# Kernel tuning notes

Measured on AMD Instinct MI355X. Metric: run time of the kernel, lower is better.

Reference implementation:

```python
import jax, jax.numpy as jnp
import numpy as np

N_NODES = 100000
N_EDGES = 1200000
EMBED_DIM = 64
N_LAYERS = 3


def setup_inputs() -> dict:
    key = jax.random.key(0)
    k1, k2, k3, k4 = jax.random.split(key, 4)
    embeddings = jax.random.normal(k1, (N_NODES, EMBED_DIM), dtype=jnp.float32)
    edge_weight = jax.random.uniform(k2, (N_EDGES,), dtype=jnp.float32)
    edge_src = jax.random.randint(k3, (N_EDGES,), 0, N_NODES, dtype=jnp.int32)
    edge_dst = jax.random.randint(k4, (N_EDGES,), 0, N_NODES, dtype=jnp.int32)
    return {"embeddings": embeddings, "edge_weight": edge_weight,
            "edge_src": edge_src, "edge_dst": edge_dst}


def _spmm(edge_src, edge_dst, edge_weight, x):
    # (A @ x)[d] = sum_{e: dst(e)=d} w[e] * x[src(e)]  -- COO SpMM via gather + segment_sum
    msgs = edge_weight[:, None] * x[edge_src]  # [E, D]
    return jax.ops.segment_sum(msgs, edge_dst, num_segments=N_NODES)


def reference(embeddings, edge_weight, edge_src, edge_dst):
    all_embeddings = [embeddings]
    ego = embeddings
    for _ in range(N_LAYERS):
        ego = _spmm(edge_src, edge_dst, edge_weight, ego)
        all_embeddings.append(ego)
    # stack layer outputs: [n_layers+1, N, D]
    return jnp.stack(all_embeddings, axis=0)
```

## Files before the change

kernel.cpp:

```cpp
#include <hip/hip_runtime.h>
#include <hip/hip_fp16.h>


#define N_NODES 100000
#define DIM 64
#define SCAN_CHUNK 1024

#define NR 8
#define RSIZE ((N_NODES + NR - 1) / NR)
#define SLICES 256

typedef int   vint4   __attribute__((ext_vector_type(4)));
typedef float vfloat4 __attribute__((ext_vector_type(4)));

union HU { unsigned u; __half2 h; };

__global__ void convert_kernel(const float* __restrict__ emb, float* __restrict__ out0,
                               unsigned short* __restrict__ xh0, int n8) {
    int i = blockIdx.x * blockDim.x + threadIdx.x;
    if (i >= n8) return;
    const vfloat4* e4 = (const vfloat4*)emb;
    vfloat4 a = __builtin_nontemporal_load(e4 + 2 * i);
    vfloat4 b = __builtin_nontemporal_load(e4 + 2 * i + 1);
    vfloat4* o4 = (vfloat4*)out0;
    __builtin_nontemporal_store(a, o4 + 2 * i);
    __builtin_nontemporal_store(b, o4 + 2 * i + 1);
    HU c0, c1, c2, c3;
    c0.h = __float22half2_rn(make_float2(a[0], a[1]));
    c1.h = __float22half2_rn(make_float2(a[2], a[3]));
    c2.h = __float22half2_rn(make_float2(b[0], b[1]));
    c3.h = __float22half2_rn(make_float2(b[2], b[3]));
    vint4 p = { (int)c0.u, (int)c1.u, (int)c2.u, (int)c3.u };
    ((vint4*)xh0)[i] = p;
}


__global__ void hist_kernel(const int* __restrict__ edst, int* __restrict__ deg, int E) {
    int i = blockIdx.x * blockDim.x + threadIdx.x;
    int nv = E >> 2;
    if (i < nv) {
        vint4 d = __builtin_nontemporal_load(((const vint4*)edst) + i);
        atomicAdd(&deg[d[0]], 1);
        atomicAdd(&deg[d[1]], 1);
        atomicAdd(&deg[d[2]], 1);
        atomicAdd(&deg[d[3]], 1);
    }
    if (i == 0) {
        for (int e = nv << 2; e < E; ++e) atomicAdd(&deg[edst[e]], 1);
    }
}

__global__ void scan1_kernel(const int* __restrict__ src, int* __restrict__ dst,
                             int* __restrict__ bsum, int n) {
    __shared__ int sdata[256];
    int tid = threadIdx.x;
    int base = blockIdx.x * SCAN_CHUNK + tid * 4;
    int v[4];
    #pragma unroll
    for (int i = 0; i < 4; ++i) v[i] = (base + i < n) ? src[base + i] : 0;
    int tsum = v[0] + v[1] + v[2] + v[3];
    sdata[tid] = tsum;
    __syncthreads();
    for (int d = 1; d < 256; d <<= 1) {
        int t = (tid >= d) ? sdata[tid - d] : 0;
        __syncthreads();
        sdata[tid] += t;
        __syncthreads();
    }
    int excl = sdata[tid] - tsum;
    if (tid == 255) bsum[blockIdx.x] = sdata[255];
    int run = excl;
    #pragma unroll
    for (int i = 0; i < 4; ++i) {
        if (base + i < n) dst[base + i] = run;
        run += v[i];
    }
}

__global__ void scan2_kernel(int* __restrict__ bsum, int nb) {
    __shared__ int s[128];
    int tid = threadIdx.x;
    int v = (tid < nb) ? bsum[tid] : 0;
    s[tid] = v;
    __syncthreads();
    for (int d = 1; d < 128; d <<= 1) {
        int t = (tid >= d) ? s[tid - d] : 0;
        __syncthreads();
        s[tid] += t;
        __syncthreads();
    }
    if (tid < nb) bsum[tid] = s[tid] - v;
}

__global__ void scan3_kernel(int* __restrict__ off, int* __restrict__ cur,
                             const int* __restrict__ bsum, int n) {
    int i = blockIdx.x * blockDim.x + threadIdx.x;
    if (i < n) {
        int v = off[i] + bsum[i / SCAN_CHUNK];
        off[i] = v;
        cur[i] = v;
    }
}

__global__ void scatter_range_kernel(const int* __restrict__ esrc, const int* __restrict__ edst,
                                     const float* __restrict__ ew, int* __restrict__ cur,
                                     int2* __restrict__ pairs, int E, int chunk) {
    const int r = blockIdx.x & (NR - 1);
    const int s = blockIdx.x / NR;
    const int lo = r * RSIZE;
    const int hi = min(lo + RSIZE, N_NODES);
    const int e0 = s * chunk;
    if (e0 >= E) return;
    const int e1 = min(e0 + chunk, E);
    const int nv = (e1 - e0) >> 2;
    const vint4*   s4 = (const vint4*)(esrc + e0);
    const vint4*   d4 = (const vint4*)(edst + e0);
    const vfloat4* w4 = (const vfloat4*)(ew + e0);
    for (int i = threadIdx.x; i < nv; i += blockDim.x) {
        vint4 dd = __builtin_nontemporal_load(d4 + i);
        vint4 ss = __builtin_nontemporal_load(s4 + i);
        vfloat4 ww = __builtin_nontemporal_load(w4 + i);
        #pragma unroll
        for (int j = 0; j < 4; ++j) {
            int dj = dd[j];
            if (dj >= lo && dj < hi) {
                int p = atomicAdd(&cur[dj], 1);
                int2 pr;
                pr.x = ss[j];
                pr.y = __float_as_int(ww[j]);
                pairs[p] = pr;
            }
        }
    }
    for (int e = e0 + (nv << 2) + threadIdx.x; e < e1; e += blockDim.x) {
        int dj = edst[e];
        if (dj >= lo && dj < hi) {
            int p = atomicAdd(&cur[dj], 1);
            int2 pr;
            pr.x = esrc[e];
            pr.y = __float_as_int(ew[e]);
            pairs[p] = pr;
        }
    }
}


__global__ void spmm_h_kernel(const unsigned short* __restrict__ xh,
                              const int2* __restrict__ pairs,
                              const int* __restrict__ off,
                              const int* __restrict__ deg,
                              float* __restrict__ y,
                              unsigned short* __restrict__ yh) {
    int gtid = blockIdx.x * blockDim.x + threadIdx.x;
    int node = gtid >> 6;
    int lane = threadIdx.x & 63;
    int o  = lane >> 3;
    int ol = lane & 7;
    if (node >= N_NODES) return;
    int s0 = off[node];
    int n  = deg[node];
    float a0 = 0.f, a1 = 0.f, a2 = 0.f, a3 = 0.f;
    float a4 = 0.f, a5 = 0.f, a6 = 0.f, a7 = 0.f;
    for (int k = o; k < n; k += 8) {
        int2 pr = pairs[s0 + k];
        float w = __int_as_float(pr.y);
        const vint4* row = (const vint4*)(xh + (size_t)pr.x * DIM);
        vint4 v = row[ol];
        HU c; float2 f;
        c.u = (unsigned)v[0]; f = __half22float2(c.h); a0 += w * f.x; a1 += w * f.y;
        c.u = (unsigned)v[1]; f = __half22float2(c.h); a2 += w * f.x; a3 += w * f.y;
        c.u = (unsigned)v[2]; f = __half22float2(c.h); a4 += w * f.x; a5 += w * f.y;
        c.u = (unsigned)v[3]; f = __half22float2(c.h); a6 += w * f.x; a7 += w * f.y;
    }
    #pragma unroll
    for (int d = 8; d <= 32; d <<= 1) {
        a0 += __shfl_xor(a0, d); a1 += __shfl_xor(a1, d);
        a2 += __shfl_xor(a2, d); a3 += __shfl_xor(a3, d);
        a4 += __shfl_xor(a4, d); a5 += __shfl_xor(a5, d);
        a6 += __shfl_xor(a6, d); a7 += __shfl_xor(a7, d);
    }
    if (o == 0) {
        float* yr = y + (size_t)node * DIM + ol * 8;
        vfloat4 r0 = { a0, a1, a2, a3 };
        vfloat4 r1 = { a4, a5, a6, a7 };
        __builtin_nontemporal_store(r0, (vfloat4*)yr);
        __builtin_nontemporal_store(r1, (vfloat4*)yr + 1);
        HU c0, c1, c2, c3;
        c0.h = __float22half2_rn(make_float2(a0, a1));
        c1.h = __float22half2_rn(make_float2(a2, a3));
        c2.h = __float22half2_rn(make_float2(a4, a5));
        c3.h = __float22half2_rn(make_float2(a6, a7));
        vint4 p = { (int)c0.u, (int)c1.u, (int)c2.u, (int)c3.u };
        *((vint4*)(yh + (size_t)node * DIM + ol * 8)) = p;
    }
}


__global__ void spmm_csr_kernel(const float* __restrict__ x,
                                const int2* __restrict__ pairs,
                                const int* __restrict__ off,
                                const int* __restrict__ deg,
                                float* __restrict__ y) {
    int gtid = blockIdx.x * blockDim.x + threadIdx.x;
    int node = gtid >> 6;
    int lane = threadIdx.x & 63;
    int o  = lane >> 3;
    int ol = lane & 7;
    if (node >= N_NODES) return;
    int s0 = off[node];
    int n  = deg[node];
    float4 a0 = make_float4(0.f, 0.f, 0.f, 0.f);
    float4 a1 = a0;
    for (int k = o; k < n; k += 8) {
        int2 pr = pairs[s0 + k];
        float w = __int_as_float(pr.y);
        const float4* row = (const float4*)(x + (size_t)pr.x * DIM);
        float4 v0 = row[ol];
        float4 v1 = row[ol + 8];
        a0.x += w * v0.x; a0.y += w * v0.y; a0.z += w * v0.z; a0.w += w * v0.w;
        a1.x += w * v1.x; a1.y += w * v1.y; a1.z += w * v1.z; a1.w += w * v1.w;
    }
    #pragma unroll
    for (int d = 8; d <= 32; d <<= 1) {
        a0.x += __shfl_xor(a0.x, d); a0.y += __shfl_xor(a0.y, d);
        a0.z += __shfl_xor(a0.z, d); a0.w += __shfl_xor(a0.w, d);
        a1.x += __shfl_xor(a1.x, d); a1.y += __shfl_xor(a1.y, d);
        a1.z += __shfl_xor(a1.z, d); a1.w += __shfl_xor(a1.w, d);
    }
    if (o == 0) {
        vfloat4* yrow = (vfloat4*)(y + (size_t)node * DIM);
        vfloat4 r0 = { a0.x, a0.y, a0.z, a0.w };
        vfloat4 r1 = { a1.x, a1.y, a1.z, a1.w };
        __builtin_nontemporal_store(r0, yrow + ol);
        __builtin_nontemporal_store(r1, yrow + ol + 8);
    }
}


__global__ void spmm_atomic_kernel(const float* __restrict__ x, const float* __restrict__ ew,
                                   const int* __restrict__ esrc, const int* __restrict__ edst,
                                   float* __restrict__ y, int n_edges) {
    long long tid = (long long)blockIdx.x * blockDim.x + threadIdx.x;
    int e = (int)(tid >> 6);
    int d = (int)(tid & 63);
    if (e >= n_edges) return;
    int s = esrc[e]; int t = edst[e]; float w = ew[e];
    atomicAdd(&y[(long long)t * DIM + d], w * x[(long long)s * DIM + d]);
}

extern "C" void kernel_launch(void* const* d_in, const int* in_sizes, int n_in,
                              void* d_out, int out_size, void* d_ws, size_t ws_size,
                              hipStream_t stream) {
    const float* emb  = (const float*)d_in[0];
    const float* ew   = (const float*)d_in[1];
    const int*   esrc = (const int*)d_in[2];
    const int*   edst = (const int*)d_in[3];
    float* out = (float*)d_out;

    const int E = in_sizes[1];
    const size_t layer_elems = (size_t)N_NODES * DIM;

    const size_t need_h   = (size_t)E * 8 + 2 * layer_elems * 2 + (size_t)3 * N_NODES * 4 + 1024;
    const size_t need_f32 = (size_t)E * 8 + (size_t)3 * N_NODES * 4 + 1024;

    if (ws_size >= need_h && E >= 4) {
        char* w = (char*)d_ws;
        int2* pairs = (int2*)w;
        unsigned short* xh0 = (unsigned short*)(w + (size_t)E * 8);
        unsigned short* xh1 = xh0 + layer_elems;
        int* deg  = (int*)(xh1 + layer_elems);
        int* cur  = deg + N_NODES;
        int* off  = cur + N_NODES;
        int* bsum = off + N_NODES;

        hipMemsetAsync(deg, 0, (size_t)N_NODES * 4, stream);

        const int n8 = (int)(layer_elems / 8);
        convert_kernel<<<(n8 + 255) / 256, 256, 0, stream>>>(emb, out, xh0, n8);

        const int nv4 = E >> 2;
        hist_kernel<<<(nv4 + 255) / 256, 256, 0, stream>>>(edst, deg, E);

        const int nscan = (N_NODES + SCAN_CHUNK - 1) / SCAN_CHUNK;
        scan1_kernel<<<nscan, 256, 0, stream>>>(deg, off, bsum, N_NODES);
        scan2_kernel<<<1, 128, 0, stream>>>(bsum, nscan);
        scan3_kernel<<<(N_NODES + 255) / 256, 256, 0, stream>>>(off, cur, bsum, N_NODES);

        const int chunk = (((E + SLICES - 1) / SLICES) + 3) & ~3;
        scatter_range_kernel<<<NR * SLICES, 256, 0, stream>>>(esrc, edst, ew, cur, pairs, E, chunk);

        const int nb = (N_NODES + 3) / 4;
        unsigned short* xs[2] = { xh0, xh1 };
        for (int l = 1; l <= 3; ++l) {
            spmm_h_kernel<<<nb, 256, 0, stream>>>(
                xs[(l - 1) & 1], pairs, off, deg,
                out + (size_t)l * layer_elems, xs[l & 1]);
        }
    } else if (ws_size >= need_f32 && E >= 4) {
        char* w = (char*)d_ws;
        int2* pairs = (int2*)w;
        int* deg  = (int*)(w + (size_t)E * 8);
        int* cur  = deg + N_NODES;
        int* off  = cur + N_NODES;
        int* bsum = off + N_NODES;

        hipMemcpyAsync(out, emb, layer_elems * sizeof(float), hipMemcpyDeviceToDevice, stream);
        hipMemsetAsync(deg, 0, (size_t)N_NODES * 4, stream);
        const int nv4 = E >> 2;
        hist_kernel<<<(nv4 + 255) / 256, 256, 0, stream>>>(edst, deg, E);
        const int nscan = (N_NODES + SCAN_CHUNK - 1) / SCAN_CHUNK;
        scan1_kernel<<<nscan, 256, 0, stream>>>(deg, off, bsum, N_NODES);
        scan2_kernel<<<1, 128, 0, stream>>>(bsum, nscan);
        scan3_kernel<<<(N_NODES + 255) / 256, 256, 0, stream>>>(off, cur, bsum, N_NODES);
        const int chunk = (((E + SLICES - 1) / SLICES) + 3) & ~3;
        scatter_range_kernel<<<NR * SLICES, 256, 0, stream>>>(esrc, edst, ew, cur, pairs, E, chunk);
        const int nb = (N_NODES + 3) / 4;
        for (int l = 1; l <= 3; ++l) {
            spmm_csr_kernel<<<nb, 256, 0, stream>>>(
                out + (size_t)(l - 1) * layer_elems, pairs, off, deg,
                out + (size_t)l * layer_elems);
        }
    } else {
        hipMemcpyAsync(out, emb, layer_elems * sizeof(float), hipMemcpyDeviceToDevice, stream);
        hipMemsetAsync(out + layer_elems, 0, 3 * layer_elems * sizeof(float), stream);
        const long long total_threads = (long long)E * 64;
        const int blocks = (int)((total_threads + 255) / 256);
        for (int l = 1; l <= 3; ++l) {
            spmm_atomic_kernel<<<blocks, 256, 0, stream>>>(
                out + (size_t)(l - 1) * layer_elems, ew, esrc, edst,
                out + (size_t)l * layer_elems, E);
        }
    }
}
```

Before: 369.9 us.

## Replace range-filtered CSR scatter with two-pass radix partition of edges

The CSR build previously had every destination-range block rescan the whole edge list, reading edges once per range. Now the histogram also records per-block range counts, those are scanned, and partA writes edges into a temp buffer bucketed by range with src and local dst packed into one word. partB then scatters each bucket into final CSR positions. This cuts redundant edge reads but adds a temp buffer, an extra pass, and a packing limit on node ids.

```diff
diff --git a/kernel.cpp b/kernel.cpp
--- a/kernel.cpp
+++ b/kernel.cpp
@@ -8,9 +8,12 @@
 
 #define NR 8
 #define RSIZE ((N_NODES + NR - 1) / NR)
+#define NBLK 256
+#define PBR 32
 #define SLICES 256
 
 typedef int   vint4   __attribute__((ext_vector_type(4)));
+typedef int   vint2   __attribute__((ext_vector_type(2)));
 typedef float vfloat4 __attribute__((ext_vector_type(4)));
 
 union HU { unsigned u; __half2 h; };
@@ -35,19 +38,33 @@
 }
 
 
-__global__ void hist_kernel(const int* __restrict__ edst, int* __restrict__ deg, int E) {
-    int i = blockIdx.x * blockDim.x + threadIdx.x;
-    int nv = E >> 2;
-    if (i < nv) {
-        vint4 d = __builtin_nontemporal_load(((const vint4*)edst) + i);
-        atomicAdd(&deg[d[0]], 1);
-        atomicAdd(&deg[d[1]], 1);
-        atomicAdd(&deg[d[2]], 1);
-        atomicAdd(&deg[d[3]], 1);
-    }
-    if (i == 0) {
-        for (int e = nv << 2; e < E; ++e) atomicAdd(&deg[edst[e]], 1);
-    }
+__global__ void hist_part_kernel(const int* __restrict__ edst, int* __restrict__ deg,
+                                 int* __restrict__ cntT, int E, int chunk) {
+    __shared__ int lcnt[NR];
+    if (threadIdx.x < NR) lcnt[threadIdx.x] = 0;
+    __syncthreads();
+    const int b = blockIdx.x;
+    const int e0 = b * chunk;
+    const int e1 = min(e0 + chunk, E);
+    if (e0 < E) {
+        const int nv = (e1 - e0) >> 2;
+        const vint4* d4 = (const vint4*)(edst + e0);
+        for (int i = threadIdx.x; i < nv; i += blockDim.x) {
+            vint4 d = __builtin_nontemporal_load(d4 + i);
+            #pragma unroll
+            for (int j = 0; j < 4; ++j) {
+                atomicAdd(&deg[d[j]], 1);
+                atomicAdd(&lcnt[d[j] / RSIZE], 1);
+            }
+        }
+        for (int e = e0 + (nv << 2) + threadIdx.x; e < e1; e += blockDim.x) {
+            int d = edst[e];
+            atomicAdd(&deg[d], 1);
+            atomicAdd(&lcnt[d / RSIZE], 1);
+        }
+    }
+    __syncthreads();
+    if (threadIdx.x < NR) cntT[threadIdx.x * NBLK + b] = lcnt[threadIdx.x];
 }
 
 __global__ void scan1_kernel(const int* __restrict__ src, int* __restrict__ dst,
@@ -77,19 +94,23 @@
     }
 }
 
-__global__ void scan2_kernel(int* __restrict__ bsum, int nb) {
-    __shared__ int s[128];
-    int tid = threadIdx.x;
-    int v = (tid < nb) ? bsum[tid] : 0;
-    s[tid] = v;
+__global__ void scan2b_kernel(int* __restrict__ a, int nb) {
+    __shared__ int s[1024];
+    int t = threadIdx.x;
+    int i0 = 2 * t, i1 = 2 * t + 1;
+    int v0 = (i0 < nb) ? a[i0] : 0;
+    int v1 = (i1 < nb) ? a[i1] : 0;
+    s[t] = v0 + v1;
     __syncthreads();
-    for (int d = 1; d < 128; d <<= 1) {
-        int t = (tid >= d) ? s[tid - d] : 0;
+    for (int d = 1; d < 1024; d <<= 1) {
+        int tt = (t >= d) ? s[t - d] : 0;
         __syncthreads();
-        s[tid] += t;
+        s[t] += tt;
         __syncthreads();
     }
-    if (tid < nb) bsum[tid] = s[tid] - v;
+    int excl = s[t] - (v0 + v1);
+    if (i0 < nb) a[i0] = excl;
+    if (i1 < nb) a[i1] = excl + v0;
 }
 
 __global__ void scan3_kernel(int* __restrict__ off, int* __restrict__ cur,
@@ -99,6 +120,138 @@
         int v = off[i] + bsum[i / SCAN_CHUNK];
         off[i] = v;
         cur[i] = v;
+    }
+}
+
+__global__ void partA_kernel(const int* __restrict__ esrc, const int* __restrict__ edst,
+                             const float* __restrict__ ew, const int* __restrict__ cntT,
+                             int2* __restrict__ tmp, int E, int chunk) {
+    __shared__ int lcur[NR];
+    const int b = blockIdx.x;
+    if (threadIdx.x < NR) lcur[threadIdx.x] = cntT[threadIdx.x * NBLK + b];
+    __syncthreads();
+    const int e0 = b * chunk;
+    if (e0 >= E) return;
+    const int e1 = min(e0 + chunk, E);
+    const int nv = (e1 - e0) >> 2;
+    const vint4*   s4 = (const vint4*)(esrc + e0);
+    const vint4*   d4 = (const vint4*)(edst + e0);
+    const vfloat4* w4 = (const vfloat4*)(ew + e0);
+    for (int i = threadIdx.x; i < nv; i += blockDim.x) {
+        vint4 dd = __builtin_nontemporal_load(d4 + i);
+        vint4 ss = __builtin_nontemporal_load(s4 + i);
+        vfloat4 ww = __builtin_nontemporal_load(w4 + i);
+        #pragma unroll
+        for (int j = 0; j < 4; ++j) {
+            int d = dd[j];
+            int r = d / RSIZE;
+            int dl = d - r * RSIZE;
+            int pos = atomicAdd(&lcur[r], 1);
+            int2 pr;
+            pr.x = ss[j] | (dl << 17);
+            pr.y = __float_as_int(ww[j]);
+            tmp[pos] = pr;
+        }
+    }
+    for (int e = e0 + (nv << 2) + threadIdx.x; e < e1; e += blockDim.x) {
+        int d = edst[e];
+        int r = d / RSIZE;
+        int dl = d - r * RSIZE;
+        int pos = atomicAdd(&lcur[r], 1);
+        int2 pr;
+        pr.x = esrc[e] | (dl << 17);
+        pr.y = __float_as_int(ew[e]);
+        tmp[pos] = pr;
+    }
+}
+
+__global__ void partB_kernel(const int2* __restrict__ tmp, const int* __restrict__ cntT,
+                             int* __restrict__ cur, int2* __restrict__ pairs, int E) {
+    const int r  = blockIdx.x & (NR - 1);
+    const int bi = blockIdx.x >> 3;
+    const int s0 = cntT[r * NBLK];
+    const int s1 = (r == NR - 1) ? E : cntT[(r + 1) * NBLK];
+    const int n  = s1 - s0;
+    const int chunk = (n + PBR - 1) / PBR;
+    const int b0 = s0 + bi * chunk;
+    const int b1 = min(b0 + chunk, s1);
+    const int rbase = r * RSIZE;
+    for (int i = b0 + threadIdx.x; i < b1; i += blockDim.x) {
+        vint2 pr = __builtin_nontemporal_load((const vint2*)(tmp + i));
+        int src = pr[0] & 0x1FFFF;
+        int dst = rbase + (int)(((unsigned)pr[0]) >> 17);
+        int p = atomicAdd(&cur[dst], 1);
+        int2 o;
+        o.x = src;
+        o.y = pr[1];
+        pairs[p] = o;
+    }
+}
+
+
+__global__ void spmm_h_kernel(const unsigned short* __restrict__ xh,
+                              const int2* __restrict__ pairs,
+                              const int* __restrict__ off,
+                              const int* __restrict__ deg,
+                              float* __restrict__ y,
+                              unsigned short* __restrict__ yh) {
+    int gtid = blockIdx.x * blockDim.x + threadIdx.x;
+    int node = gtid >> 6;
+    int lane = threadIdx.x & 63;
+    int o  = lane >> 3;
+    int ol = lane & 7;
+    if (node >= N_NODES) return;
+    int s0 = off[node];
+    int n  = deg[node];
+    float a0 = 0.f, a1 = 0.f, a2 = 0.f, a3 = 0.f;
+    float a4 = 0.f, a5 = 0.f, a6 = 0.f, a7 = 0.f;
+    for (int k = o; k < n; k += 8) {
+        int2 pr = pairs[s0 + k];
+        float w = __int_as_float(pr.y);
+        const vint4* row = (const vint4*)(xh + (size_t)pr.x * DIM);
+        vint4 v = row[ol];
+        HU c; float2 f;
+        c.u = (unsigned)v[0]; f = __half22float2(c.h); a0 += w * f.x; a1 += w * f.y;
+        c.u = (unsigned)v[1]; f = __half22float2(c.h); a2 += w * f.x; a3 += w * f.y;
+        c.u = (unsigned)v[2]; f = __half22float2(c.h); a4 += w * f.x; a5 += w * f.y;
+        c.u = (unsigned)v[3]; f = __half22float2(c.h); a6 += w * f.x; a7 += w * f.y;
+    }
+    #pragma unroll
+    for (int d = 8; d <= 32; d <<= 1) {
+        a0 += __shfl_xor(a0, d); a1 += __shfl_xor(a1, d);
+        a2 += __shfl_xor(a2, d); a3 += __shfl_xor(a3, d);
+        a4 += __shfl_xor(a4, d); a5 += __shfl_xor(a5, d);
+        a6 += __shfl_xor(a6, d); a7 += __shfl_xor(a7, d);
+    }
+    if (o == 0) {
+        float* yr = y + (size_t)node * DIM + ol * 8;
+        vfloat4 r0 = { a0, a1, a2, a3 };
+        vfloat4 r1 = { a4, a5, a6, a7 };
+        __builtin_nontemporal_store(r0, (vfloat4*)yr);
+        __builtin_nontemporal_store(r1, (vfloat4*)yr + 1);
+        HU c0, c1, c2, c3;
+        c0.h = __float22half2_rn(make_float2(a0, a1));
+        c1.h = __float22half2_rn(make_float2(a2, a3));
+        c2.h = __float22half2_rn(make_float2(a4, a5));
+        c3.h = __float22half2_rn(make_float2(a6, a7));
+        vint4 p = { (int)c0.u, (int)c1.u, (int)c2.u, (int)c3.u };
+        *((vint4*)(yh + (size_t)node * DIM + ol * 8)) = p;
+    }
+}
+
+
+__global__ void hist_kernel(const int* __restrict__ edst, int* __restrict__ deg, int E) {
+    int i = blockIdx.x * blockDim.x + threadIdx.x;
+    int nv = E >> 2;
+    if (i < nv) {
+        vint4 d = __builtin_nontemporal_load(((const vint4*)edst) + i);
+        atomicAdd(&deg[d[0]], 1);
+        atomicAdd(&deg[d[1]], 1);
+        atomicAdd(&deg[d[2]], 1);
+        atomicAdd(&deg[d[3]], 1);
+    }
+    if (i == 0) {
+        for (int e = nv << 2; e < E; ++e) atomicAdd(&deg[edst[e]], 1);
     }
 }
 
@@ -144,58 +297,6 @@
     }
 }
 
-
-__global__ void spmm_h_kernel(const unsigned short* __restrict__ xh,
-                              const int2* __restrict__ pairs,
-                              const int* __restrict__ off,
-                              const int* __restrict__ deg,
-                              float* __restrict__ y,
-                              unsigned short* __restrict__ yh) {
-    int gtid = blockIdx.x * blockDim.x + threadIdx.x;
-    int node = gtid >> 6;
-    int lane = threadIdx.x & 63;
-    int o  = lane >> 3;
-    int ol = lane & 7;
-    if (node >= N_NODES) return;
-    int s0 = off[node];
-    int n  = deg[node];
-    float a0 = 0.f, a1 = 0.f, a2 = 0.f, a3 = 0.f;
-    float a4 = 0.f, a5 = 0.f, a6 = 0.f, a7 = 0.f;
-    for (int k = o; k < n; k += 8) {
-        int2 pr = pairs[s0 + k];
-        float w = __int_as_float(pr.y);
-        const vint4* row = (const vint4*)(xh + (size_t)pr.x * DIM);
-        vint4 v = row[ol];
-        HU c; float2 f;
-        c.u = (unsigned)v[0]; f = __half22float2(c.h); a0 += w * f.x; a1 += w * f.y;
-        c.u = (unsigned)v[1]; f = __half22float2(c.h); a2 += w * f.x; a3 += w * f.y;
-        c.u = (unsigned)v[2]; f = __half22float2(c.h); a4 += w * f.x; a5 += w * f.y;
-        c.u = (unsigned)v[3]; f = __half22float2(c.h); a6 += w * f.x; a7 += w * f.y;
-    }
-    #pragma unroll
-    for (int d = 8; d <= 32; d <<= 1) {
-        a0 += __shfl_xor(a0, d); a1 += __shfl_xor(a1, d);
-        a2 += __shfl_xor(a2, d); a3 += __shfl_xor(a3, d);
-        a4 += __shfl_xor(a4, d); a5 += __shfl_xor(a5, d);
-        a6 += __shfl_xor(a6, d); a7 += __shfl_xor(a7, d);
-    }
-    if (o == 0) {
-        float* yr = y + (size_t)node * DIM + ol * 8;
-        vfloat4 r0 = { a0, a1, a2, a3 };
-        vfloat4 r1 = { a4, a5, a6, a7 };
-        __builtin_nontemporal_store(r0, (vfloat4*)yr);
-        __builtin_nontemporal_store(r1, (vfloat4*)yr + 1);
-        HU c0, c1, c2, c3;
-        c0.h = __float22half2_rn(make_float2(a0, a1));
-        c1.h = __float22half2_rn(make_float2(a2, a3));
-        c2.h = __float22half2_rn(make_float2(a4, a5));
-        c3.h = __float22half2_rn(make_float2(a6, a7));
-        vint4 p = { (int)c0.u, (int)c1.u, (int)c2.u, (int)c3.u };
-        *((vint4*)(yh + (size_t)node * DIM + ol * 8)) = p;
-    }
-}
-
-
 __global__ void spmm_csr_kernel(const float* __restrict__ x,
                                 const int2* __restrict__ pairs,
                                 const int* __restrict__ off,
@@ -236,7 +337,6 @@
     }
 }
 
-
 __global__ void spmm_atomic_kernel(const float* __restrict__ x, const float* __restrict__ ew,
                                    const int* __restrict__ esrc, const int* __restrict__ edst,
                                    float* __restrict__ y, int n_edges) {
@@ -260,34 +360,40 @@
     const int E = in_sizes[1];
     const size_t layer_elems = (size_t)N_NODES * DIM;
 
-    const size_t need_h   = (size_t)E * 8 + 2 * layer_elems * 2 + (size_t)3 * N_NODES * 4 + 1024;
+    const size_t need_new = (size_t)E * 16 + 2 * layer_elems * 2
+                          + (size_t)3 * N_NODES * 4 + (size_t)(NBLK * NR + 1024) * 4 + 1024;
     const size_t need_f32 = (size_t)E * 8 + (size_t)3 * N_NODES * 4 + 1024;
 
-    if (ws_size >= need_h && E >= 4) {
+
+    if (ws_size >= need_new && E >= 4) {
         char* w = (char*)d_ws;
         int2* pairs = (int2*)w;
-        unsigned short* xh0 = (unsigned short*)(w + (size_t)E * 8);
+        int2* tmp   = (int2*)(w + (size_t)E * 8);
+        unsigned short* xh0 = (unsigned short*)(w + (size_t)E * 16);
         unsigned short* xh1 = xh0 + layer_elems;
         int* deg  = (int*)(xh1 + layer_elems);
         int* cur  = deg + N_NODES;
         int* off  = cur + N_NODES;
-        int* bsum = off + N_NODES;
+        int* cntT = off + N_NODES;
+        int* bsum = cntT + NBLK * NR;
 
         hipMemsetAsync(deg, 0, (size_t)N_NODES * 4, stream);
 
         const int n8 = (int)(layer_elems / 8);
         convert_kernel<<<(n8 + 255) / 256, 256, 0, stream>>>(emb, out, xh0, n8);
 
-        const int nv4 = E >> 2;
-        hist_kernel<<<(nv4 + 255) / 256, 256, 0, stream>>>(edst, deg, E);
+        const int pchunk = (((E + NBLK - 1) / NBLK) + 3) & ~3;
+        hist_part_kernel<<<NBLK, 256, 0, stream>>>(edst, deg, cntT, E, pchunk);
 
         const int nscan = (N_NODES + SCAN_CHUNK - 1) / SCAN_CHUNK;
         scan1_kernel<<<nscan, 256, 0, stream>>>(deg, off, bsum, N_NODES);
-        scan2_kernel<<<1, 128, 0, stream>>>(bsum, nscan);
+        scan2b_kernel<<<1, 1024, 0, stream>>>(bsum, nscan);
         scan3_kernel<<<(N_NODES + 255) / 256, 256, 0, stream>>>(off, cur, bsum, N_NODES);
 
-        const int chunk = (((E + SLICES - 1) / SLICES) + 3) & ~3;
-        scatter_range_kernel<<<NR * SLICES, 256, 0, stream>>>(esrc, edst, ew, cur, pairs, E, chunk);
+        scan2b_kernel<<<1, 1024, 0, stream>>>(cntT, NBLK * NR);
+
+        partA_kernel<<<NBLK, 256, 0, stream>>>(esrc, edst, ew, cntT, tmp, E, pchunk);
+        partB_kernel<<<NR * PBR, 256, 0, stream>>>(tmp, cntT, cur, pairs, E);
 
         const int nb = (N_NODES + 3) / 4;
         unsigned short* xs[2] = { xh0, xh1 };
@@ -310,7 +416,7 @@
         hist_kernel<<<(nv4 + 255) / 256, 256, 0, stream>>>(edst, deg, E);
         const int nscan = (N_NODES + SCAN_CHUNK - 1) / SCAN_CHUNK;
         scan1_kernel<<<nscan, 256, 0, stream>>>(deg, off, bsum, N_NODES);
-        scan2_kernel<<<1, 128, 0, stream>>>(bsum, nscan);
+        scan2b_kernel<<<1, 1024, 0, stream>>>(bsum, nscan);
         scan3_kernel<<<(N_NODES + 255) / 256, 256, 0, stream>>>(off, cur, bsum, N_NODES);
         const int chunk = (((E + SLICES - 1) / SLICES) + 3) & ~3;
         scatter_range_kernel<<<NR * SLICES, 256, 0, stream>>>(esrc, edst, ew, cur, pairs, E, chunk);
```

Measured after the change: 372.9 us. Within noise of the previous version (+0.8%).
